# Optimization experiments

Measured on AMD Instinct MI355X. Metric: run time of the kernel, lower is better.

The kernel has to match this reference:

```python
import jax, jax.numpy as jnp
import numpy as np

B, N, D = 4, 1024, 64
H, DH = 8, 64
INNER = H * DH  # 512 == dim*heads
NUM_F, GH, GW = 4, 16, 16  # N = GH*GW*NUM_F
EPS_LN = 1e-5


def setup_inputs() -> dict:
    key = jax.random.key(0)
    ks = jax.random.split(key, 5)
    return {
        "x": jax.random.normal(ks[0], (B, N, D), dtype=jnp.float32),
        "W_qkv": jax.random.normal(ks[1], (D, 3 * INNER), dtype=jnp.float32) * 0.05,
        "b_qkv": jax.random.normal(ks[2], (3 * INNER,), dtype=jnp.float32) * 0.02,
        "ln_g": jnp.ones((INNER,), dtype=jnp.float32),
        "ln_b": jnp.zeros((INNER,), dtype=jnp.float32),
        "W_out": jax.random.normal(ks[3], (INNER, D), dtype=jnp.float32) * 0.05,
        "b_out": jnp.zeros((D,), dtype=jnp.float32),
    }


def _safe_sqrt(d2):
    # sqrt with zero (not inf) gradient at 0 (diagonal of cdist)
    pos = d2 > 1e-12
    return jnp.where(pos, jnp.sqrt(jnp.where(pos, d2, 1.0)), 0.0)


def _spe_weights(x):
    # torch.cdist(x, x, p=2) then Gaussian kernel, thresholded at mean
    sq = jnp.sum(x * x, axis=-1)  # (B,N)
    d2 = sq[:, :, None] + sq[:, None, :] - 2.0 * jnp.einsum('bnd,bmd->bnm', x, x)
    d2 = jnp.maximum(d2, 0.0)
    dist = _safe_sqrt(d2)
    sigma = jnp.mean(dist)
    w = jnp.exp(-d2 / (2.0 * sigma * sigma))
    return jnp.where(w < jnp.mean(w), 0.0, w)  # (B,N,N)


def _spa_weights():
    # constant spatial-grid Gaussian weights, identical across batch
    gx, gy, gz = jnp.meshgrid(jnp.arange(GH), jnp.arange(GW), jnp.arange(NUM_F), indexing='ij')
    grid = jnp.stack([gx, gy, gz], axis=-1).reshape(N, 3).astype(jnp.float32)
    diff = grid[:, None, :] - grid[None, :, :]
    d2 = jnp.sum(diff * diff, axis=-1)
    dist = jnp.sqrt(d2)
    sigma = jnp.mean(dist)
    w = jnp.exp(-d2 / (2.0 * sigma * sigma))
    return jnp.where(w < jnp.mean(w), 0.0, w)  # (N,N)


def reference(x, W_qkv, b_qkv, ln_g, ln_b, W_out, b_out):
    spe = _spe_weights(x)            # (B,N,N), broadcast over heads
    spa = _spa_weights()             # (N,N), broadcast over batch & heads

    qkv = x @ W_qkv + b_qkv          # (B,N,3*INNER)
    q, k, v = jnp.split(qkv, 3, axis=-1)
    to_heads = lambda t: t.reshape(B, N, H, DH).transpose(0, 2, 1, 3)  # (B,H,N,DH)
    q, k, v = to_heads(q), to_heads(k), to_heads(v)

    scale = DH ** (-0.5)
    qe = jax.nn.elu(q) + 1.0
    ke = jax.nn.elu(k) + 1.0
    dots = jnp.einsum('bhid,bhjd->bhij', qe, ke) * scale  # (B,H,N,N)

    masked = dots * spe[:, None, :, :] * spa[None, None, :, :]
    attn = jax.nn.softmax(masked, axis=-1)
    out = jnp.einsum('bhij,bhjd->bhid', attn, v)          # (B,H,N,DH)
    out = out.transpose(0, 2, 1, 3).reshape(B, N, INNER)

    # to_out: LayerNorm -> GELU (exact) -> Linear
    mu = jnp.mean(out, axis=-1, keepdims=True)
    var = jnp.var(out, axis=-1, keepdims=True)
    y = ln_g * (out - mu) / jnp.sqrt(var + EPS_LN) + ln_b
    y = jax.nn.gelu(y, approximate=False)
    return y @ W_out + b_out  # (B,N,D)
```

## Files before the change

kernel.cpp:

```cpp
#include <hip/hip_runtime.h>
#include <math.h>
#include <stdlib.h>

#define B 4
#define N 1024
#define D 64
#define H 8
#define DH 64
#define INNER 512
#define C3 1536
#define BHN 32768
#define BHND 2097152

typedef __attribute__((ext_vector_type(8))) short bf16x8;
typedef __attribute__((ext_vector_type(4))) float f32x4;

__device__ inline short f2bf(float f) {
    unsigned u = __builtin_bit_cast(unsigned, f);
    unsigned r = (u + 0x7FFFu + ((u >> 16) & 1u)) >> 16;
    return (short)r;
}
__device__ inline float bf2f(short s) {
    return __builtin_bit_cast(float, ((unsigned)(unsigned short)s) << 16);
}

__global__ __launch_bounds__(256) void k_prep(const float* __restrict__ x, const float* __restrict__ Wqkv,
                                              short* __restrict__ xh, short* __restrict__ xl,
                                              float* __restrict__ sq,
                                              short* __restrict__ Wh, short* __restrict__ Wl,
                                              float* __restrict__ spa, float inv2s2, float mu,
                                              float* __restrict__ scal) {
    __shared__ float lds[64 * 65];
    int t = threadIdx.x;
    int bb = blockIdx.x;
    if (bb < 1024) {
        if (bb == 0 && t < 16) scal[t] = 0.f;
        int i = bb * 4 + (t >> 6), d = t & 63;
        float v = x[i * 64 + d];
        short hs = f2bf(v);
        xh[i * 64 + d] = hs;
        xl[i * 64 + d] = f2bf(v - bf2f(hs));
        float s = v * v;
#pragma unroll
        for (int m = 32; m; m >>= 1) s += __shfl_xor(s, m, 64);
        if (d == 0) sq[i] = s;
    } else if (bb < 1048) {
        int c0 = (bb - 1024) * 64;
#pragma unroll
        for (int it = 0; it < 16; it++) {
            int d = it * 4 + (t >> 6), cl = t & 63;
            lds[cl * 65 + d] = Wqkv[d * C3 + c0 + cl];
        }
        __syncthreads();
#pragma unroll
        for (int it = 0; it < 16; it++) {
            int cl = it * 4 + (t >> 6), d = t & 63;
            float v = lds[cl * 65 + d];
            short hs = f2bf(v);
            Wh[(c0 + cl) * 64 + d] = hs;
            Wl[(c0 + cl) * 64 + d] = f2bf(v - bf2f(hs));
        }
    } else {
        int flat4 = (bb - 1048) * 256 + t;
        int i = flat4 >> 8;
        int j0 = (flat4 & 255) * 4;
        int ix = i >> 6, iy = (i >> 2) & 15, iz = i & 3;
        float4 o;
        float* op = (float*)&o;
#pragma unroll
        for (int jj = 0; jj < 4; jj++) {
            int j = j0 + jj;
            int jx = j >> 6, jy = (j >> 2) & 15, jz = j & 3;
            float d2 = (float)((ix - jx) * (ix - jx) + (iy - jy) * (iy - jy) + (iz - jz) * (iz - jz));
            float w = __expf(-d2 * inv2s2);
            op[jj] = (w < mu) ? 0.f : w;
        }
        ((float4*)spa)[flat4] = o;
    }
}

__global__ __launch_bounds__(256) void k_gemm(
    const short* __restrict__ xh, const short* __restrict__ xl,
    const short* __restrict__ Wh, const short* __restrict__ Wl,
    const float* __restrict__ bqkv, const float* __restrict__ sq,
    short* __restrict__ qeh, short* __restrict__ qel,
    short* __restrict__ keh, short* __restrict__ kel,
    short* __restrict__ vT, float* __restrict__ w, float* __restrict__ d_sig) {
    __shared__ short vt_lds[128 * 66];
    __shared__ float red[4];
    int t = threadIdx.x;
    int wv = t >> 6, lane = t & 63, l4 = lane & 15, g = lane >> 4;
    const bf16x8* xh8 = (const bf16x8*)xh;
    const bf16x8* xl8 = (const bf16x8*)xl;

    if (blockIdx.x < 768) {
        int i0 = (blockIdx.x & 63) * 64;
        int c0 = (blockIdx.x >> 6) * 128;
        int irow = i0 + wv * 16;
        const bf16x8* Wh8 = (const bf16x8*)Wh;
        const bf16x8* Wl8 = (const bf16x8*)Wl;
        int abase = (irow + l4) * 8 + g;
        bf16x8 ah[2], al[2];
        ah[0] = xh8[abase];
        ah[1] = xh8[abase + 4];
        al[0] = xl8[abase];
        al[1] = xl8[abase + 4];
        f32x4 acc[8];
#pragma unroll
        for (int ct = 0; ct < 8; ct++) {
            int c = c0 + 16 * ct + l4;
            int bbase = c * 8 + g;
            bf16x8 bh0 = Wh8[bbase], bh1 = Wh8[bbase + 4];
            bf16x8 bl0 = Wl8[bbase], bl1 = Wl8[bbase + 4];
            f32x4 a = f32x4{0.f, 0.f, 0.f, 0.f};
            a = __builtin_amdgcn_mfma_f32_16x16x32_bf16(ah[0], bh0, a, 0, 0, 0);
            a = __builtin_amdgcn_mfma_f32_16x16x32_bf16(ah[1], bh1, a, 0, 0, 0);
            a = __builtin_amdgcn_mfma_f32_16x16x32_bf16(al[0], bh0, a, 0, 0, 0);
            a = __builtin_amdgcn_mfma_f32_16x16x32_bf16(al[1], bh1, a, 0, 0, 0);
            a = __builtin_amdgcn_mfma_f32_16x16x32_bf16(ah[0], bl0, a, 0, 0, 0);
            a = __builtin_amdgcn_mfma_f32_16x16x32_bf16(ah[1], bl1, a, 0, 0, 0);
            acc[ct] = a;
        }
        int seg = c0 >> 9;
#pragma unroll
        for (int ct = 0; ct < 8; ct++) {
            int c = c0 + 16 * ct + l4;
            float bias = bqkv[c];
            int cc = c & 511, hh = cc >> 6, dh = cc & 63;
#pragma unroll
            for (int r = 0; r < 4; r++) {
                int i_e = irow + 4 * g + r;
                int b = i_e >> 10, i = i_e & 1023;
                float val = acc[ct][r] + bias;
                if (seg < 2) {
                    float a_ = val > 0.f ? val + 1.f : __expf(val);
                    short hs = f2bf(a_);
                    short ls = f2bf(a_ - bf2f(hs));
                    int off = ((b * H + hh) * N + i) * 64 + dh;
                    if (seg == 0) { qeh[off] = hs; qel[off] = ls; }
                    else          { keh[off] = hs; kel[off] = ls; }
                } else {
                    vt_lds[(16 * ct + l4) * 66 + (wv * 16 + 4 * g + r)] = f2bf(val);
                }
            }
        }
        if (seg == 2) {
            __syncthreads();
            int b = i0 >> 10, ib = i0 & 1023;
#pragma unroll
            for (int it = 0; it < 4; it++) {
                int idx = t + 256 * it;
                int cl = idx >> 3, i8 = idx & 7;
                short tmp[8];
#pragma unroll
                for (int r8 = 0; r8 < 8; r8++) tmp[r8] = vt_lds[cl * 66 + i8 * 8 + r8];
                int cc = (c0 + cl) & 511, hh = cc >> 6, dh = cc & 63;
                ((bf16x8*)vT)[((b * H + hh) * 64 + dh) * (N / 8) + (ib >> 3) + i8] = *(bf16x8*)tmp;
            }
        }
    } else {
        int q = blockIdx.x - 768;
        int i0 = (q & 15) * 64, j0 = ((q >> 4) & 7) * 128, b = q >> 7;
        int irow = i0 + wv * 16;
        int abase = (b * N + irow + l4) * 8 + g;
        bf16x8 ah[2], al[2];
        ah[0] = xh8[abase];
        ah[1] = xh8[abase + 4];
        al[0] = xl8[abase];
        al[1] = xl8[abase + 4];
        f32x4 acc[8];
#pragma unroll
        for (int ct = 0; ct < 8; ct++) {
            int j = j0 + 16 * ct + l4;
            int bbase = (b * N + j) * 8 + g;
            bf16x8 bh0 = xh8[bbase], bh1 = xh8[bbase + 4];
            bf16x8 bl0 = xl8[bbase], bl1 = xl8[bbase + 4];
            f32x4 a = f32x4{0.f, 0.f, 0.f, 0.f};
            a = __builtin_amdgcn_mfma_f32_16x16x32_bf16(ah[0], bh0, a, 0, 0, 0);
            a = __builtin_amdgcn_mfma_f32_16x16x32_bf16(ah[1], bh1, a, 0, 0, 0);
            a = __builtin_amdgcn_mfma_f32_16x16x32_bf16(al[0], bh0, a, 0, 0, 0);
            a = __builtin_amdgcn_mfma_f32_16x16x32_bf16(al[1], bh1, a, 0, 0, 0);
            a = __builtin_amdgcn_mfma_f32_16x16x32_bf16(ah[0], bl0, a, 0, 0, 0);
            a = __builtin_amdgcn_mfma_f32_16x16x32_bf16(ah[1], bl1, a, 0, 0, 0);
            acc[ct] = a;
        }
        float sqi[4];
#pragma unroll
        for (int r = 0; r < 4; r++) sqi[r] = sq[b * N + irow + 4 * g + r];
        float part = 0.f;
#pragma unroll
        for (int ct = 0; ct < 8; ct++) {
            int j = j0 + 16 * ct + l4;
            float sqj = sq[b * N + j];
#pragma unroll
            for (int r = 0; r < 4; r++) {
                float d2 = sqi[r] + sqj - 2.f * acc[ct][r];
                d2 = fmaxf(d2, 0.f);
                w[((size_t)b * N + irow + 4 * g + r) * N + j] = d2;
                part += (d2 > 1e-12f) ? sqrtf(d2) : 0.f;
            }
        }
#pragma unroll
        for (int m = 32; m; m >>= 1) part += __shfl_xor(part, m, 64);
        if (lane == 0) red[wv] = part;
        __syncthreads();
        if (t == 0) atomicAdd(d_sig, red[0] + red[1] + red[2] + red[3]);
    }
}

__global__ __launch_bounds__(256) void k_wsum(const float* __restrict__ w, const float* __restrict__ d_sig,
                                              float* __restrict__ d_wsum) {
    __shared__ float red[4];
    float sigma = d_sig[0] * (1.f / 4194304.f);
    float inv = 1.f / (2.f * sigma * sigma);
    float s = 0.f;
    for (int idx = blockIdx.x * 256 + threadIdx.x; idx < 1048576; idx += 256 * 2048) {
        float4 v = ((const float4*)w)[idx];
        s += __expf(-v.x * inv) + __expf(-v.y * inv) + __expf(-v.z * inv) + __expf(-v.w * inv);
    }
#pragma unroll
    for (int m = 32; m; m >>= 1) s += __shfl_xor(s, m, 64);
    if ((threadIdx.x & 63) == 0) red[threadIdx.x >> 6] = s;
    __syncthreads();
    if (threadIdx.x == 0) atomicAdd(d_wsum, red[0] + red[1] + red[2] + red[3]);
}

__global__ __launch_bounds__(256) void k_mask(const float* __restrict__ w, const float* __restrict__ spa,
                                              const float* __restrict__ scal, short* __restrict__ Mb) {
    float sigma = scal[0] * (1.f / 4194304.f);
    float inv = 1.f / (2.f * sigma * sigma);
    float mu = scal[1] * (1.f / 4194304.f);
    float d2thr = -__logf(mu) / inv;
    for (int idx = blockIdx.x * 256 + threadIdx.x; idx < 1048576; idx += 256 * 2048) {
        float4 d2v = ((const float4*)w)[idx];
        float4 sp = ((const float4*)spa)[idx & 262143];
        short tmp[4];
        float* dp = (float*)&d2v;
        float* pp = (float*)&sp;
#pragma unroll
        for (int e = 0; e < 4; e++) {
            float m = (dp[e] > d2thr) ? 0.f : __expf(-dp[e] * inv) * pp[e] * 0.125f;
            tmp[e] = f2bf(m);
        }
        *(uint2*)(Mb + (size_t)idx * 4) = *(uint2*)tmp;
    }
}

__global__ __launch_bounds__(256) void k_attn(
    const short* __restrict__ qeh, const short* __restrict__ qel,
    const short* __restrict__ keh, const short* __restrict__ kel,
    const short* __restrict__ vT, const short* __restrict__ Mb,
    float* __restrict__ aout) {
    __shared__ short Kh[64 * 64];
    __shared__ short Kl[64 * 64];
    __shared__ short Vt[64 * 64];
    __shared__ short P[4][16 * 64];
    int t = threadIdx.x;
    int wv = t >> 6, lane = t & 63, l4 = lane & 15, g = lane >> 4;
    int i0 = blockIdx.x * 64;
    int h = blockIdx.y, b = blockIdx.z, bh = b * H + h;
    int irow = i0 + wv * 16;

    bf16x8 qh[2], ql[2];
    {
        const bf16x8* qh8 = (const bf16x8*)qeh;
        const bf16x8* ql8 = (const bf16x8*)qel;
        int base = (bh * N + irow + l4) * 8 + g;
#pragma unroll
        for (int mk = 0; mk < 2; mk++) {
            qh[mk] = qh8[base + 4 * mk];
            ql[mk] = ql8[base + 4 * mk];
        }
    }
    f32x4 O[4];
#pragma unroll
    for (int dt = 0; dt < 4; dt++) O[dt] = f32x4{0.f, 0.f, 0.f, 0.f};
    float m_r[4] = {-INFINITY, -INFINITY, -INFINITY, -INFINITY};
    float l_r[4] = {0.f, 0.f, 0.f, 0.f};

    const bf16x8* Kh8 = (const bf16x8*)Kh;
    const bf16x8* Kl8 = (const bf16x8*)Kl;
    const bf16x8* Vt8 = (const bf16x8*)Vt;

    for (int tile = 0; tile < 16; ++tile) {
        int j0 = tile * 64;
        __syncthreads();
        {
            const bf16x8* kh8 = (const bf16x8*)keh;
            const bf16x8* kl8 = (const bf16x8*)kel;
            const bf16x8* v8 = (const bf16x8*)vT;
            bf16x8* KhW = (bf16x8*)Kh;
            bf16x8* KlW = (bf16x8*)Kl;
            bf16x8* VtW = (bf16x8*)Vt;
#pragma unroll
            for (int rep = 0; rep < 2; rep++) {
                int c = t + 256 * rep;
                int j = c >> 3, s = c & 7;
                KhW[j * 8 + (s ^ (j & 7))] = kh8[(bh * N + j0 + j) * 8 + s];
                KlW[j * 8 + (s ^ (j & 7))] = kl8[(bh * N + j0 + j) * 8 + s];
                VtW[j * 8 + (s ^ (j & 7))] = v8[(bh * 64 + j) * (N / 8) + (j0 >> 3) + s];
            }
        }
        __syncthreads();
        f32x4 sc[4];
        __builtin_amdgcn_s_setprio(1);
#pragma unroll
        for (int ct = 0; ct < 4; ct++) {
            int j = 16 * ct + l4;
            int sw = j & 7;
            bf16x8 kh0 = Kh8[j * 8 + ((g) ^ sw)];
            bf16x8 kh1 = Kh8[j * 8 + ((4 + g) ^ sw)];
            bf16x8 kl0 = Kl8[j * 8 + ((g) ^ sw)];
            bf16x8 kl1 = Kl8[j * 8 + ((4 + g) ^ sw)];
            f32x4 a = f32x4{0.f, 0.f, 0.f, 0.f};
            a = __builtin_amdgcn_mfma_f32_16x16x32_bf16(qh[0], kh0, a, 0, 0, 0);
            a = __builtin_amdgcn_mfma_f32_16x16x32_bf16(qh[1], kh1, a, 0, 0, 0);
            a = __builtin_amdgcn_mfma_f32_16x16x32_bf16(ql[0], kh0, a, 0, 0, 0);
            a = __builtin_amdgcn_mfma_f32_16x16x32_bf16(ql[1], kh1, a, 0, 0, 0);
            a = __builtin_amdgcn_mfma_f32_16x16x32_bf16(qh[0], kl0, a, 0, 0, 0);
            a = __builtin_amdgcn_mfma_f32_16x16x32_bf16(qh[1], kl1, a, 0, 0, 0);
            sc[ct] = a;
        }
        __builtin_amdgcn_s_setprio(0);
        float p[4][4];
        float fr[4];
#pragma unroll
        for (int r = 0; r < 4; r++) {
            int i = irow + 4 * g + r;
            const short* Mrow = Mb + ((size_t)b * N + i) * N + j0;
            float mx = -INFINITY;
#pragma unroll
            for (int ct = 0; ct < 4; ct++) {
                float mval = bf2f(Mrow[16 * ct + l4]);
                float val = sc[ct][r] * mval;
                p[ct][r] = val;
                mx = fmaxf(mx, val);
            }
#pragma unroll
            for (int msk = 1; msk < 16; msk <<= 1) mx = fmaxf(mx, __shfl_xor(mx, msk, 64));
            float mo = m_r[r];
            float mn = fmaxf(mo, mx);
            float f = __expf(mo - mn);
            float s = 0.f;
#pragma unroll
            for (int ct = 0; ct < 4; ct++) {
                float e = __expf(p[ct][r] - mn);
                p[ct][r] = e;
                s += e;
            }
#pragma unroll
            for (int msk = 1; msk < 16; msk <<= 1) s += __shfl_xor(s, msk, 64);
            l_r[r] = l_r[r] * f + s;
            m_r[r] = mn;
            fr[r] = f;
        }
#pragma unroll
        for (int dt = 0; dt < 4; dt++) {
            O[dt][0] *= fr[0];
            O[dt][1] *= fr[1];
            O[dt][2] *= fr[2];
            O[dt][3] *= fr[3];
        }
        short* Pw = P[wv];
#pragma unroll
        for (int ct = 0; ct < 4; ct++) {
#pragma unroll
            for (int r = 0; r < 4; r++) {
                int row = 4 * g + r;
                int slot = ((l4 >> 3) + 2 * ct) ^ (row & 7);
                Pw[row * 64 + slot * 8 + (l4 & 7)] = f2bf(p[ct][r]);
            }
        }
        const bf16x8* Pr = (const bf16x8*)P[wv];
        __builtin_amdgcn_s_setprio(1);
#pragma unroll
        for (int ks = 0; ks < 2; ks++) {
            bf16x8 pa = Pr[l4 * 8 + ((g + 4 * ks) ^ (l4 & 7))];
#pragma unroll
            for (int dt = 0; dt < 4; dt++) {
                int d = l4 + 16 * dt;
                bf16x8 bv = Vt8[d * 8 + ((g + 4 * ks) ^ (d & 7))];
                O[dt] = __builtin_amdgcn_mfma_f32_16x16x32_bf16(pa, bv, O[dt], 0, 0, 0);
            }
        }
        __builtin_amdgcn_s_setprio(0);
    }
#pragma unroll
    for (int dt = 0; dt < 4; dt++) {
#pragma unroll
        for (int r = 0; r < 4; r++) {
            int i = irow + 4 * g + r;
            aout[((size_t)b * N + i) * INNER + h * 64 + l4 + 16 * dt] = O[dt][r] / l_r[r];
        }
    }
}

__global__ __launch_bounds__(256) void k_out(const float* __restrict__ aout, const float* __restrict__ g,
                                             const float* __restrict__ be, const float* __restrict__ Wout,
                                             const float* __restrict__ bout, float* __restrict__ out) {
    __shared__ float y_s[8 * 512];
    int t = threadIdx.x;
    int wv = t >> 6, lane = t & 63;
    int r0 = blockIdx.x * 8;
#pragma unroll
    for (int rr = 0; rr < 2; rr++) {
        int rloc = wv * 2 + rr;
        const float* rp = aout + (size_t)(r0 + rloc) * 512;
        float4 v0 = ((const float4*)rp)[lane];
        float4 v1 = ((const float4*)rp)[lane + 64];
        float s1 = v0.x + v0.y + v0.z + v0.w + v1.x + v1.y + v1.z + v1.w;
        float s2 = v0.x * v0.x + v0.y * v0.y + v0.z * v0.z + v0.w * v0.w +
                   v1.x * v1.x + v1.y * v1.y + v1.z * v1.z + v1.w * v1.w;
#pragma unroll
        for (int m = 32; m; m >>= 1) {
            s1 += __shfl_xor(s1, m, 64);
            s2 += __shfl_xor(s2, m, 64);
        }
        float mean = s1 * (1.f / 512.f);
        float var = s2 * (1.f / 512.f) - mean * mean;
        float rstd = rsqrtf(var + 1e-5f);
        int c0 = 4 * lane, c1 = 4 * lane + 256;
        float4 o0, o1;
#pragma unroll
        for (int e = 0; e < 4; e++) {
            float yn = g[c0 + e] * (((float*)&v0)[e] - mean) * rstd + be[c0 + e];
            ((float*)&o0)[e] = 0.5f * yn * (1.f + erff(yn * 0.70710678118f));
            float ym = g[c1 + e] * (((float*)&v1)[e] - mean) * rstd + be[c1 + e];
            ((float*)&o1)[e] = 0.5f * ym * (1.f + erff(ym * 0.70710678118f));
        }
        ((float4*)(y_s + rloc * 512))[lane] = o0;
        ((float4*)(y_s + rloc * 512))[lane + 64] = o1;
    }
    __syncthreads();
    int o = t & 63, rg = t >> 6;
    float a0 = 0.f, a1 = 0.f;
#pragma unroll 4
    for (int c = 0; c < 512; c++) {
        float wv_ = Wout[c * 64 + o];
        a0 = fmaf(y_s[(rg * 2) * 512 + c], wv_, a0);
        a1 = fmaf(y_s[(rg * 2 + 1) * 512 + c], wv_, a1);
    }
    float bo = bout[o];
    out[(size_t)(r0 + rg * 2) * 64 + o] = a0 + bo;
    out[(size_t)(r0 + rg * 2 + 1) * 64 + o] = a1 + bo;
}

extern "C" void kernel_launch(void* const* d_in, const int* in_sizes, int n_in,
                              void* d_out, int out_size, void* d_ws, size_t ws_size,
                              hipStream_t stream) {
    const float* x = (const float*)d_in[0];
    const float* Wqkv = (const float*)d_in[1];
    const float* bqkv = (const float*)d_in[2];
    const float* lng = (const float*)d_in[3];
    const float* lnb = (const float*)d_in[4];
    const float* Wout = (const float*)d_in[5];
    const float* bout = (const float*)d_in[6];
    float* out = (float*)d_out;

    float* ws = (float*)d_ws;
    size_t off = 0;
    float* sq = ws + off;    off += (size_t)B * N;
    float* scal = ws + off;  off += 16;
    float* spa = ws + off;   off += (size_t)N * N;
    float* wbuf = ws + off;  off += (size_t)B * N * N;
    float* aout = ws + off;  off += (size_t)B * N * INNER;
    short* sbase = (short*)(ws + off);
    size_t soff = 0;
    short* qeh = sbase + soff; soff += (size_t)BHND;
    short* qel = sbase + soff; soff += (size_t)BHND;
    short* keh = sbase + soff; soff += (size_t)BHND;
    short* kel = sbase + soff; soff += (size_t)BHND;
    short* vT  = sbase + soff; soff += (size_t)BHND;
    short* Mb  = sbase + soff; soff += (size_t)B * N * N;
    short* xh  = sbase + soff; soff += (size_t)B * N * D;
    short* xl  = sbase + soff; soff += (size_t)B * N * D;
    short* Wh  = sbase + soff; soff += (size_t)D * C3;
    short* Wl  = sbase + soff; soff += (size_t)D * C3;

    double ssum = 0.0;
    const double cnt = (double)N * (double)N;
    for (int dx = -15; dx <= 15; dx++)
        for (int dy = -15; dy <= 15; dy++)
            for (int dz = -3; dz <= 3; dz++) {
                double c = (double)(16 - abs(dx)) * (double)(16 - abs(dy)) * (double)(4 - abs(dz));
                double d2 = (double)(dx * dx + dy * dy + dz * dz);
                ssum += c * sqrt(d2);
            }
    double sigma = ssum / cnt;
    double inv2s2 = 1.0 / (2.0 * sigma * sigma);
    double wsum = 0.0;
    for (int dx = -15; dx <= 15; dx++)
        for (int dy = -15; dy <= 15; dy++)
            for (int dz = -3; dz <= 3; dz++) {
                double c = (double)(16 - abs(dx)) * (double)(16 - abs(dy)) * (double)(4 - abs(dz));
                double d2 = (double)(dx * dx + dy * dy + dz * dz);
                wsum += c * exp(-d2 * inv2s2);
            }
    double mu = wsum / cnt;

    k_prep<<<2072, 256, 0, stream>>>(x, Wqkv, xh, xl, sq, Wh, Wl, spa, (float)inv2s2, (float)mu, scal);
    k_gemm<<<1280, 256, 0, stream>>>(xh, xl, Wh, Wl, bqkv, sq, qeh, qel, keh, kel, vT, wbuf, scal);
    k_wsum<<<2048, 256, 0, stream>>>(wbuf, scal, scal + 1);
    k_mask<<<2048, 256, 0, stream>>>(wbuf, spa, scal, Mb);
    k_attn<<<dim3(N / 64, H, B), 256, 0, stream>>>(qeh, qel, keh, kel, vT, Mb, aout);
    k_out<<<512, 256, 0, stream>>>(aout, lng, lnb, Wout, bout, out);
}
```

Before: 221.9 us.

## Drop K low-part split and double-buffer K/V tiles in attention

Stops producing and consuming the low bf16 residual of K, which cuts two of six MFMAs per score tile along with a full buffer of global writes and reads. The attention loop now double-buffers K and V in LDS, prefetching tile t+2 into registers while computing tile t, and uses one barrier per tile. The grid is flattened with heads as the fastest-varying index, likely to improve L2 reuse of the mask tile. Score precision is lower because K is only a single bf16 while Q keeps its hi/lo split.

```diff
diff --git a/kernel.cpp b/kernel.cpp
--- a/kernel.cpp
+++ b/kernel.cpp
@@ -84,7 +84,7 @@
     const short* __restrict__ Wh, const short* __restrict__ Wl,
     const float* __restrict__ bqkv, const float* __restrict__ sq,
     short* __restrict__ qeh, short* __restrict__ qel,
-    short* __restrict__ keh, short* __restrict__ kel,
+    short* __restrict__ keh,
     short* __restrict__ vT, float* __restrict__ w, float* __restrict__ d_sig) {
     __shared__ short vt_lds[128 * 66];
     __shared__ float red[4];
@@ -135,10 +135,13 @@
                 if (seg < 2) {
                     float a_ = val > 0.f ? val + 1.f : __expf(val);
                     short hs = f2bf(a_);
-                    short ls = f2bf(a_ - bf2f(hs));
                     int off = ((b * H + hh) * N + i) * 64 + dh;
-                    if (seg == 0) { qeh[off] = hs; qel[off] = ls; }
-                    else          { keh[off] = hs; kel[off] = ls; }
+                    if (seg == 0) {
+                        qeh[off] = hs;
+                        qel[off] = f2bf(a_ - bf2f(hs));
+                    } else {
+                        keh[off] = hs;
+                    }
                 } else {
                     vt_lds[(16 * ct + l4) * 66 + (wv * 16 + 4 * g + r)] = f2bf(val);
                 }
@@ -248,17 +251,20 @@
 
 __global__ __launch_bounds__(256) void k_attn(
     const short* __restrict__ qeh, const short* __restrict__ qel,
-    const short* __restrict__ keh, const short* __restrict__ kel,
+    const short* __restrict__ keh,
     const short* __restrict__ vT, const short* __restrict__ Mb,
     float* __restrict__ aout) {
-    __shared__ short Kh[64 * 64];
-    __shared__ short Kl[64 * 64];
-    __shared__ short Vt[64 * 64];
+    __shared__ short Kh[2][64 * 64];
+    __shared__ short Vt[2][64 * 64];
     __shared__ short P[4][16 * 64];
     int t = threadIdx.x;
     int wv = t >> 6, lane = t & 63, l4 = lane & 15, g = lane >> 4;
-    int i0 = blockIdx.x * 64;
-    int h = blockIdx.y, b = blockIdx.z, bh = b * H + h;
+    int bid = blockIdx.x;
+    int h = bid & 7;
+    int iblk = (bid >> 3) & 15;
+    int b = bid >> 7;
+    int i0 = iblk * 64;
+    int bh = b * H + h;
     int irow = i0 + wv * 16;
 
     bf16x8 qh[2], ql[2];
@@ -278,30 +284,41 @@
     float m_r[4] = {-INFINITY, -INFINITY, -INFINITY, -INFINITY};
     float l_r[4] = {0.f, 0.f, 0.f, 0.f};
 
-    const bf16x8* Kh8 = (const bf16x8*)Kh;
-    const bf16x8* Kl8 = (const bf16x8*)Kl;
-    const bf16x8* Vt8 = (const bf16x8*)Vt;
+    const bf16x8* kh8 = (const bf16x8*)keh;
+    const bf16x8* v8 = (const bf16x8*)vT;
+    int j_a = (t + 0) >> 3, s_a = (t + 0) & 7;
+    int j_b = (t + 256) >> 3, s_b = (t + 256) & 7;
+
+    bf16x8 rk[2], rv[2];
+#define LOAD_T(T)                                                            \
+    {                                                                        \
+        int j0_ = (T) * 64;                                                  \
+        rk[0] = kh8[(bh * N + j0_ + j_a) * 8 + s_a];                         \
+        rk[1] = kh8[(bh * N + j0_ + j_b) * 8 + s_b];                         \
+        rv[0] = v8[(bh * 64 + j_a) * (N / 8) + (j0_ >> 3) + s_a];            \
+        rv[1] = v8[(bh * 64 + j_b) * (N / 8) + (j0_ >> 3) + s_b];            \
+    }
+#define STORE_T(BUF)                                                         \
+    {                                                                        \
+        ((bf16x8*)Kh[BUF])[j_a * 8 + (s_a ^ (j_a & 7))] = rk[0];             \
+        ((bf16x8*)Kh[BUF])[j_b * 8 + (s_b ^ (j_b & 7))] = rk[1];             \
+        ((bf16x8*)Vt[BUF])[j_a * 8 + (s_a ^ (j_a & 7))] = rv[0];             \
+        ((bf16x8*)Vt[BUF])[j_b * 8 + (s_b ^ (j_b & 7))] = rv[1];             \
+    }
+
+    LOAD_T(0);
+    STORE_T(0);
+    LOAD_T(1);
+    __syncthreads();
 
     for (int tile = 0; tile < 16; ++tile) {
+        int cur = tile & 1, nxt = cur ^ 1;
         int j0 = tile * 64;
-        __syncthreads();
-        {
-            const bf16x8* kh8 = (const bf16x8*)keh;
-            const bf16x8* kl8 = (const bf16x8*)kel;
-            const bf16x8* v8 = (const bf16x8*)vT;
-            bf16x8* KhW = (bf16x8*)Kh;
-            bf16x8* KlW = (bf16x8*)Kl;
-            bf16x8* VtW = (bf16x8*)Vt;
-#pragma unroll
-            for (int rep = 0; rep < 2; rep++) {
-                int c = t + 256 * rep;
-                int j = c >> 3, s = c & 7;
-                KhW[j * 8 + (s ^ (j & 7))] = kh8[(bh * N + j0 + j) * 8 + s];
-                KlW[j * 8 + (s ^ (j & 7))] = kl8[(bh * N + j0 + j) * 8 + s];
-                VtW[j * 8 + (s ^ (j & 7))] = v8[(bh * 64 + j) * (N / 8) + (j0 >> 3) + s];
-            }
-        }
-        __syncthreads();
+        if (tile < 15) STORE_T(nxt);
+        if (tile < 14) LOAD_T(tile + 2);
+
+        const bf16x8* Kh8 = (const bf16x8*)Kh[cur];
+        const bf16x8* Vt8 = (const bf16x8*)Vt[cur];
         f32x4 sc[4];
         __builtin_amdgcn_s_setprio(1);
 #pragma unroll
@@ -310,15 +327,11 @@
             int sw = j & 7;
             bf16x8 kh0 = Kh8[j * 8 + ((g) ^ sw)];
             bf16x8 kh1 = Kh8[j * 8 + ((4 + g) ^ sw)];
-            bf16x8 kl0 = Kl8[j * 8 + ((g) ^ sw)];
-            bf16x8 kl1 = Kl8[j * 8 + ((4 + g) ^ sw)];
             f32x4 a = f32x4{0.f, 0.f, 0.f, 0.f};
             a = __builtin_amdgcn_mfma_f32_16x16x32_bf16(qh[0], kh0, a, 0, 0, 0);
             a = __builtin_amdgcn_mfma_f32_16x16x32_bf16(qh[1], kh1, a, 0, 0, 0);
             a = __builtin_amdgcn_mfma_f32_16x16x32_bf16(ql[0], kh0, a, 0, 0, 0);
             a = __builtin_amdgcn_mfma_f32_16x16x32_bf16(ql[1], kh1, a, 0, 0, 0);
-            a = __builtin_amdgcn_mfma_f32_16x16x32_bf16(qh[0], kl0, a, 0, 0, 0);
-            a = __builtin_amdgcn_mfma_f32_16x16x32_bf16(qh[1], kl1, a, 0, 0, 0);
             sc[ct] = a;
         }
         __builtin_amdgcn_s_setprio(0);
@@ -384,6 +397,7 @@
             }
         }
         __builtin_amdgcn_s_setprio(0);
+        __syncthreads();
     }
 #pragma unroll
     for (int dt = 0; dt < 4; dt++) {
@@ -393,6 +407,8 @@
             aout[((size_t)b * N + i) * INNER + h * 64 + l4 + 16 * dt] = O[dt][r] / l_r[r];
         }
     }
+#undef LOAD_T
+#undef STORE_T
 }
 
 __global__ __launch_bounds__(256) void k_out(const float* __restrict__ aout, const float* __restrict__ g,
@@ -469,7 +485,6 @@
     short* qeh = sbase + soff; soff += (size_t)BHND;
     short* qel = sbase + soff; soff += (size_t)BHND;
     short* keh = sbase + soff; soff += (size_t)BHND;
-    short* kel = sbase + soff; soff += (size_t)BHND;
     short* vT  = sbase + soff; soff += (size_t)BHND;
     short* Mb  = sbase + soff; soff += (size_t)B * N * N;
     short* xh  = sbase + soff; soff += (size_t)B * N * D;
@@ -499,9 +514,9 @@
     double mu = wsum / cnt;
 
     k_prep<<<2072, 256, 0, stream>>>(x, Wqkv, xh, xl, sq, Wh, Wl, spa, (float)inv2s2, (float)mu, scal);
-    k_gemm<<<1280, 256, 0, stream>>>(xh, xl, Wh, Wl, bqkv, sq, qeh, qel, keh, kel, vT, wbuf, scal);
+    k_gemm<<<1280, 256, 0, stream>>>(xh, xl, Wh, Wl, bqkv, sq, qeh, qel, keh, vT, wbuf, scal);
     k_wsum<<<2048, 256, 0, stream>>>(wbuf, scal, scal + 1);
     k_mask<<<2048, 256, 0, stream>>>(wbuf, spa, scal, Mb);
-    k_attn<<<dim3(N / 64, H, B), 256, 0, stream>>>(qeh, qel, keh, kel, vT, Mb, aout);
+    k_attn<<<512, 256, 0, stream>>>(qeh, qel, keh, vT, Mb, aout);
     k_out<<<512, 256, 0, stream>>>(aout, lng, lnb, Wout, bout, out);
 }
```

Measured after the change: 233.4 us. +5.2%, slower.
